# Performance work log

Measured on AMD Instinct MI355X. Metric: run time of the kernel, lower is better.

The kernel has to match this reference:

```python
import jax, jax.numpy as jnp
import numpy as np

# Complete 8-ary tree, depth 5 (levels 0..5), nodes stored level-major.
C = 8
DEPTH = 5
E = 64
H = 512
VOCAB = 20
SIZES = [C ** d for d in range(DEPTH + 1)]
OFFSETS = np.concatenate([[0], np.cumsum(SIZES)]).tolist()
TOTAL = OFFSETS[-1]  # 37449


def setup_inputs() -> dict:
    key = jax.random.key(0)
    ks = jax.random.split(key, 8)
    node_types = jax.random.randint(ks[0], (TOTAL,), 0, 19, dtype=jnp.int32)
    emb = jax.random.normal(ks[1], (VOCAB, E), jnp.float32)
    s_c = 1.0 / np.sqrt(E + H)
    s_g = 1.0 / np.sqrt(H)
    Wc_w = jax.random.normal(ks[2], (H, E + H), jnp.float32) * s_c
    Wc_b = jax.random.normal(ks[3], (H,), jnp.float32) * s_c
    W_ih = jax.random.normal(ks[4], (3 * H, H), jnp.float32) * s_g
    W_hh = jax.random.normal(ks[5], (3 * H, H), jnp.float32) * s_g
    b_ih = jax.random.normal(ks[6], (3 * H,), jnp.float32) * s_g
    b_hh = jax.random.normal(ks[7], (3 * H,), jnp.float32) * s_g
    return {"node_types": node_types, "emb": emb, "Wc_w": Wc_w, "Wc_b": Wc_b,
            "W_ih": W_ih, "W_hh": W_hh, "b_ih": b_ih, "b_hh": b_hh}


def _gru_last(seq, W_ih, W_hh, b_ih, b_hh):
    """PyTorch-convention GRU over child axis; seq: [n, C, H] -> last hidden [n, H]."""
    n = seq.shape[0]
    gx = jnp.einsum('ncH,gH->cng', seq, W_ih) + b_ih  # [C, n, 3H], precomputed input gates

    def step(h, gx_t):
        gh = h @ W_hh.T + b_hh
        xr, xz, xn = jnp.split(gx_t, 3, axis=-1)
        hr, hz, hn = jnp.split(gh, 3, axis=-1)
        r = jax.nn.sigmoid(xr + hr)
        z = jax.nn.sigmoid(xz + hz)
        cand = jnp.tanh(xn + r * hn)
        h_new = (1.0 - z) * cand + z * h
        return h_new, None

    h0 = jnp.zeros((n, H), seq.dtype)
    h_last, _ = jax.lax.scan(step, h0, gx)
    return h_last


def reference(node_types, emb, Wc_w, Wc_b, W_ih, W_hh, b_ih, b_hh):
    embeds = emb[node_types]                       # [TOTAL, E]
    Wc_e = Wc_w[:, :E]                              # acts on embedding part
    Wc_h = Wc_w[:, E:]                              # acts on child-encoding part
    # Leaf level: hidden part of concat is zero-padded -> only Wc_e contributes.
    off = OFFSETS[DEPTH]
    h = jnp.tanh(embeds[off:off + SIZES[DEPTH]] @ Wc_e.T + Wc_b)  # [8^5, H]
    # Bottom-up level batching: each internal node's children are contiguous.
    for d in range(DEPTH - 1, -1, -1):
        child_seq = h.reshape(SIZES[d], C, H)
        child_enc = _gru_last(child_seq, W_ih, W_hh, b_ih, b_hh)  # [8^d, H]
        off = OFFSETS[d]
        h = jnp.tanh(embeds[off:off + SIZES[d]] @ Wc_e.T + child_enc @ Wc_h.T + Wc_b)
    return h[0]  # root encoding, [H]
```

## Files before the change

kernel.cpp:

```cpp
#include <hip/hip_runtime.h>
#include <hip/hip_bf16.h>
#include <math.h>

#define HID 512
#define WCW_LD 576
#define LEAF 4681

typedef unsigned short u16;
typedef __attribute__((ext_vector_type(8))) short bf16x8;
typedef __attribute__((ext_vector_type(4))) float f32x4;

__device__ __forceinline__ u16 f2bf(float f) {
    union { float f; unsigned u; } x; x.f = f;
    unsigned r = x.u + 0x7fffu + ((x.u >> 16) & 1u);
    return (u16)(r >> 16);
}
__device__ __forceinline__ float bf2f(u16 b) {
    union { unsigned u; float f; } x; x.u = ((unsigned)b) << 16; return x.f;
}
__device__ __forceinline__ float sigm(float x) { return 1.f / (1.f + expf(-x)); }

__device__ __forceinline__ int swz(int row, int byte) { return byte ^ ((row & 7) << 4); }

__global__ void pe_kernel(const float* __restrict__ emb, const float* __restrict__ Wc_w,
                          const float* __restrict__ Wc_b, float* __restrict__ Pe,
                          u16* __restrict__ PeT16) {
    int v = blockIdx.x, j = threadIdx.x;
    __shared__ float e[64];
    if (threadIdx.x < 64) e[threadIdx.x] = emb[v * 64 + threadIdx.x];
    __syncthreads();
    float acc = Wc_b[j];
    const float* w = Wc_w + (long long)j * WCW_LD;
#pragma unroll 8
    for (int k = 0; k < 64; ++k) acc += e[k] * w[k];
    Pe[v * HID + j] = acc;
    PeT16[v * HID + j] = f2bf(tanhf(acc));
}

__global__ void conv_w_kernel(const float* __restrict__ W_ih, const float* __restrict__ W_hh,
                              const float* __restrict__ Wc_w,
                              u16* __restrict__ Wih16, u16* __restrict__ Whh16,
                              u16* __restrict__ Wch16) {
    int idx = blockIdx.x * blockDim.x + threadIdx.x;
    int stride = gridDim.x * blockDim.x;
    for (int i = idx; i < 3 * HID * HID; i += stride) {
        Wih16[i] = f2bf(W_ih[i]);
        Whh16[i] = f2bf(W_hh[i]);
    }
    for (int i = idx; i < HID * HID; i += stride) {
        int j = i >> 9, k = i & 511;
        Wch16[i] = f2bf(Wc_w[(long long)j * WCW_LD + 64 + k]);
    }
}

__global__ __launch_bounds__(256)
void gx20_kernel(const u16* __restrict__ PeT16, const u16* __restrict__ Wih16,
                 const float* __restrict__ b_ih, float* __restrict__ Gx20) {
    int v = blockIdx.x;
    int j = blockIdx.y * 256 + threadIdx.x;
    const u16* a = PeT16 + v * HID;
    const u16* b = Wih16 + (long long)j * HID;
    float acc = b_ih[j];
    for (int k = 0; k < HID; k += 8) {
        bf16x8 av = *(const bf16x8*)(a + k);
        bf16x8 bv = *(const bf16x8*)(b + k);
#pragma unroll
        for (int i = 0; i < 8; ++i) acc += bf2f((u16)av[i]) * bf2f((u16)bv[i]);
    }
    Gx20[v * 1536 + j] = acc;
}

__global__ void h1_kernel(const float* __restrict__ Gx20, const float* __restrict__ b_hh,
                          float* __restrict__ H1f, u16* __restrict__ H1_16) {
    int v = blockIdx.x, j = threadIdx.x;
    float xr = Gx20[v * 1536 + j], xz = Gx20[v * 1536 + 512 + j], xn = Gx20[v * 1536 + 1024 + j];
    float r = sigm(xr + b_hh[j]);
    float z = sigm(xz + b_hh[HID + j]);
    float cand = tanhf(xn + r * b_hh[2 * HID + j]);
    float h = (1.f - z) * cand;
    H1f[v * HID + j] = h;
    H1_16[v * HID + j] = f2bf(h);
}

template<bool F32OUT>
__global__ __launch_bounds__(256)
void gx_gemm(const u16* __restrict__ Asrc, const u16* __restrict__ W16,
             const float* __restrict__ bias, u16* __restrict__ g16,
             float* __restrict__ gf, int M) {
    __shared__ __align__(16) uint8_t sA[128 * 128];
    __shared__ __align__(16) uint8_t sB[64 * 128];
    int tid = threadIdx.x, lane = tid & 63, w = tid >> 6;
    int j0 = blockIdx.x * 64;
    int m0 = blockIdx.y * 128;

    f32x4 acc[2][4];
#pragma unroll
    for (int m = 0; m < 2; ++m)
#pragma unroll
        for (int jf = 0; jf < 4; ++jf) acc[m][jf] = (f32x4){0.f, 0.f, 0.f, 0.f};

    for (int k0 = 0; k0 < HID; k0 += 64) {
#pragma unroll
        for (int l = 0; l < 4; ++l) {
            int e = tid + l * 256;
            int r = e >> 3, c = e & 7;
            int gm = m0 + r;
            uint4 v = make_uint4(0u, 0u, 0u, 0u);
            if (gm < M) v = *(const uint4*)(Asrc + (long long)gm * HID + k0 + c * 8);
            *(uint4*)(sA + r * 128 + swz(r, c * 16)) = v;
        }
#pragma unroll
        for (int l = 0; l < 2; ++l) {
            int e = tid + l * 256;
            int r = e >> 3, c = e & 7;
            uint4 v = *(const uint4*)(W16 + (long long)(j0 + r) * HID + k0 + c * 8);
            *(uint4*)(sB + r * 128 + swz(r, c * 16)) = v;
        }
        __syncthreads();
#pragma unroll
        for (int ks = 0; ks < 2; ++ks) {
            int kb = ks * 64 + ((lane >> 4) << 4);
            int ar = lane & 15;
            bf16x8 a0 = *(const bf16x8*)(sA + (w * 32 + ar) * 128 + swz(ar, kb));
            bf16x8 a1 = *(const bf16x8*)(sA + (w * 32 + 16 + ar) * 128 + swz(ar, kb));
#pragma unroll
            for (int jf = 0; jf < 4; ++jf) {
                bf16x8 b = *(const bf16x8*)(sB + (jf * 16 + ar) * 128 + swz(ar, kb));
                acc[0][jf] = __builtin_amdgcn_mfma_f32_16x16x32_bf16(a0, b, acc[0][jf], 0, 0, 0);
                acc[1][jf] = __builtin_amdgcn_mfma_f32_16x16x32_bf16(a1, b, acc[1][jf], 0, 0, 0);
            }
        }
        __syncthreads();
    }

#pragma unroll
    for (int jf = 0; jf < 4; ++jf) {
        int j = j0 + jf * 16 + (lane & 15);
        float bv = bias[j];
#pragma unroll
        for (int m = 0; m < 2; ++m) {
#pragma unroll
            for (int q = 0; q < 4; ++q) {
                int row = m0 + w * 32 + m * 16 + (lane >> 4) * 4 + q;
                if (row < M) {
                    float val = acc[m][jf][q] + bv;
                    if (F32OUT) gf[(long long)row * 1536 + j] = val;
                    else        g16[(long long)row * 1536 + j] = f2bf(val);
                }
            }
        }
    }
}

__global__ __launch_bounds__(256)
void h2_expand(const float* __restrict__ Gx20, const float* __restrict__ Gh1,
               const float* __restrict__ H1f, float* __restrict__ h2f,
               u16* __restrict__ h2_16) {
    int idx = blockIdx.x * 256 + threadIdx.x;
    int pr = idx >> 9, j = idx & 511;
    int v0 = pr / 20, v1 = pr % 20;
    const float* gx = Gx20 + (long long)v1 * 1536 + j;
    const float* gh = Gh1 + (long long)v0 * 1536 + j;
    float r = sigm(gx[0] + gh[0]);
    float z = sigm(gx[512] + gh[512]);
    float cand = tanhf(gx[1024] + r * gh[1024]);
    float h = (1.f - z) * cand + z * H1f[(long long)v0 * HID + j];
    h2f[(long long)pr * HID + j] = h;
    h2_16[(long long)pr * HID + j] = f2bf(h);
}

__global__ __launch_bounds__(256)
void h3_expand(const float* __restrict__ Gx20, const float* __restrict__ Gh2,
               const float* __restrict__ h2f, const int* __restrict__ nt,
               float* __restrict__ hdst_f, u16* __restrict__ hdst16) {
    int idx = blockIdx.x * 256 + threadIdx.x;
    int p = idx >> 9, j = idx & 511;
    int v0 = nt[LEAF + p * 8], v1 = nt[LEAF + p * 8 + 1], v2 = nt[LEAF + p * 8 + 2];
    int pr = v0 * 20 + v1;
    const float* gx = Gx20 + (long long)v2 * 1536 + j;
    const float* gh = Gh2 + (long long)pr * 1536 + j;
    float r = sigm(gx[0] + gh[0]);
    float z = sigm(gx[512] + gh[512]);
    float cand = tanhf(gx[1024] + r * gh[1024]);
    float h = (1.f - z) * cand + z * h2f[(long long)pr * HID + j];
    hdst_f[(long long)p * HID + j] = h;
    hdst16[(long long)p * HID + j] = f2bf(h);
}

template<int GX_TABLE>
__global__ __launch_bounds__(256, 4)
void step32(const u16* __restrict__ hsrc16, const float* __restrict__ hsrc_f,
            const float* __restrict__ Gx20, const u16* __restrict__ gx16, int t,
            const int* __restrict__ nt,
            float* __restrict__ hdst_f, u16* __restrict__ hdst16,
            const u16* __restrict__ Whh16, const float* __restrict__ b_hh, int n) {
    __shared__ __align__(16) uint8_t sA[32 * 128];
    __shared__ __align__(16) uint8_t sB[3][64 * 128];
    int tid = threadIdx.x, lane = tid & 63, w = tid >> 6;
    int p0 = blockIdx.x * 32, j0 = blockIdx.y * 64;
    int ar = lane & 15;

    f32x4 acc[3][2];
#pragma unroll
    for (int g = 0; g < 3; ++g)
#pragma unroll
        for (int m = 0; m < 2; ++m) acc[g][m] = (f32x4){0.f, 0.f, 0.f, 0.f};

    for (int kt = 0; kt < 8; ++kt) {
        int k0 = kt * 64;
        {
            int r = tid >> 3, c = tid & 7;
            int p = p0 + r;
            uint4 v = make_uint4(0u, 0u, 0u, 0u);
            if (p < n) v = *(const uint4*)(hsrc16 + (long long)p * HID + k0 + c * 8);
            *(uint4*)(sA + r * 128 + swz(r, c * 16)) = v;
        }
#pragma unroll
        for (int g = 0; g < 3; ++g) {
#pragma unroll
            for (int l = 0; l < 2; ++l) {
                int e = tid + l * 256;
                int r = e >> 3, c = e & 7;
                uint4 v = *(const uint4*)(Whh16 + (long long)(g * HID + j0 + r) * HID + k0 + c * 8);
                *(uint4*)(sB[g] + r * 128 + swz(r, c * 16)) = v;
            }
        }
        __syncthreads();
#pragma unroll
        for (int ks = 0; ks < 2; ++ks) {
            int kb = ks * 64 + ((lane >> 4) << 4);
            bf16x8 a0 = *(const bf16x8*)(sA + ar * 128 + swz(ar, kb));
            bf16x8 a1 = *(const bf16x8*)(sA + (16 + ar) * 128 + swz(ar, kb));
#pragma unroll
            for (int g = 0; g < 3; ++g) {
                bf16x8 b = *(const bf16x8*)(sB[g] + (w * 16 + ar) * 128 + swz(ar, kb));
                acc[g][0] = __builtin_amdgcn_mfma_f32_16x16x32_bf16(a0, b, acc[g][0], 0, 0, 0);
                acc[g][1] = __builtin_amdgcn_mfma_f32_16x16x32_bf16(a1, b, acc[g][1], 0, 0, 0);
            }
        }
        __syncthreads();
    }

    int jj = j0 + w * 16 + ar;
    float bhr = b_hh[jj], bhz = b_hh[HID + jj], bhn = b_hh[2 * HID + jj];
#pragma unroll
    for (int m = 0; m < 2; ++m) {
#pragma unroll
        for (int q = 0; q < 4; ++q) {
            int p = p0 + m * 16 + (lane >> 4) * 4 + q;
            if (p >= n) continue;
            float xr, xz, xn;
            if (GX_TABLE) {
                int v = nt[LEAF + p * 8 + t];
                const float* gp = Gx20 + (long long)v * 1536 + jj;
                xr = gp[0]; xz = gp[512]; xn = gp[1024];
            } else {
                long long gb = ((long long)(p * 8 + t)) * 1536 + jj;
                xr = bf2f(gx16[gb]); xz = bf2f(gx16[gb + 512]); xn = bf2f(gx16[gb + 1024]);
            }
            float r = sigm(xr + acc[0][m][q] + bhr);
            float z = sigm(xz + acc[1][m][q] + bhz);
            float cand = tanhf(xn + r * (acc[2][m][q] + bhn));
            float hp = hsrc_f[(long long)p * HID + jj];
            float hnew = (1.f - z) * cand + z * hp;
            hdst_f[(long long)p * HID + jj] = hnew;
            hdst16[(long long)p * HID + jj] = f2bf(hnew);
        }
    }
}

__global__ __launch_bounds__(256, 4)
void combine32(const u16* __restrict__ enc_in, const u16* __restrict__ Wch16,
               const int* __restrict__ nt, int off, const float* __restrict__ Pe,
               u16* __restrict__ out16, int n) {
    __shared__ __align__(16) uint8_t sA[32 * 128];
    __shared__ __align__(16) uint8_t sB[64 * 128];
    int tid = threadIdx.x, lane = tid & 63, w = tid >> 6;
    int p0 = blockIdx.x * 32, j0 = blockIdx.y * 64;
    int ar = lane & 15;

    f32x4 acc[2];
    acc[0] = (f32x4){0.f, 0.f, 0.f, 0.f};
    acc[1] = (f32x4){0.f, 0.f, 0.f, 0.f};

    for (int kt = 0; kt < 8; ++kt) {
        int k0 = kt * 64;
        {
            int r = tid >> 3, c = tid & 7;
            uint4 v = make_uint4(0u, 0u, 0u, 0u);
            if (p0 + r < n) v = *(const uint4*)(enc_in + (long long)(p0 + r) * HID + k0 + c * 8);
            *(uint4*)(sA + r * 128 + swz(r, c * 16)) = v;
        }
#pragma unroll
        for (int l = 0; l < 2; ++l) {
            int e = tid + l * 256;
            int r = e >> 3, c = e & 7;
            uint4 v = *(const uint4*)(Wch16 + (long long)(j0 + r) * HID + k0 + c * 8);
            *(uint4*)(sB + r * 128 + swz(r, c * 16)) = v;
        }
        __syncthreads();
#pragma unroll
        for (int ks = 0; ks < 2; ++ks) {
            int kb = ks * 64 + ((lane >> 4) << 4);
            bf16x8 a0 = *(const bf16x8*)(sA + ar * 128 + swz(ar, kb));
            bf16x8 a1 = *(const bf16x8*)(sA + (16 + ar) * 128 + swz(ar, kb));
            bf16x8 b = *(const bf16x8*)(sB + (w * 16 + ar) * 128 + swz(ar, kb));
            acc[0] = __builtin_amdgcn_mfma_f32_16x16x32_bf16(a0, b, acc[0], 0, 0, 0);
            acc[1] = __builtin_amdgcn_mfma_f32_16x16x32_bf16(a1, b, acc[1], 0, 0, 0);
        }
        __syncthreads();
    }

    int jj = j0 + w * 16 + ar;
#pragma unroll
    for (int m = 0; m < 2; ++m) {
#pragma unroll
        for (int q = 0; q < 4; ++q) {
            int p = p0 + m * 16 + (lane >> 4) * 4 + q;
            if (p >= n) continue;
            int tv = nt[off + p];
            float v = tanhf(Pe[(long long)tv * HID + jj] + acc[m][q]);
            out16[(long long)p * HID + jj] = f2bf(v);
        }
    }
}

__global__ __launch_bounds__(256)
void t0_simt(const u16* __restrict__ gx16, const float* __restrict__ b_hh,
             float* __restrict__ hdst_f, u16* __restrict__ hdst16, int n) {
    int idx = blockIdx.x * 256 + threadIdx.x;
    int p = idx >> 9, j = idx & 511;
    if (p >= n) return;
    long long gb = ((long long)(p * 8)) * 1536 + j;
    float xr = bf2f(gx16[gb]), xz = bf2f(gx16[gb + 512]), xn = bf2f(gx16[gb + 1024]);
    float r = sigm(xr + b_hh[j]);
    float z = sigm(xz + b_hh[HID + j]);
    float cand = tanhf(xn + r * b_hh[2 * HID + j]);
    float h = (1.f - z) * cand;
    hdst_f[(long long)p * HID + j] = h;
    hdst16[(long long)p * HID + j] = f2bf(h);
}

__global__ __launch_bounds__(256)
void step_simt(const u16* __restrict__ gx16, int t,
               const float* __restrict__ hsrc_f, const u16* __restrict__ hsrc16,
               float* __restrict__ hdst_f, u16* __restrict__ hdst16,
               const u16* __restrict__ Whh16, const float* __restrict__ b_hh, int n) {
    int idx = blockIdx.x * 256 + threadIdx.x;
    int kc = idx & 3, pj = idx >> 2;
    int p = pj >> 9, j = pj & 511;
    if (p >= n) return;
    const u16* hp16 = hsrc16 + (long long)p * HID + kc * 128;
    const u16* w0 = Whh16 + (long long)j * HID + kc * 128;
    const u16* w1 = w0 + (long long)HID * HID;
    const u16* w2 = w1 + (long long)HID * HID;
    float a0 = 0.f, a1 = 0.f, a2 = 0.f;
#pragma unroll 4
    for (int k = 0; k < 128; k += 8) {
        bf16x8 hv = *(const bf16x8*)(hp16 + k);
        bf16x8 v0 = *(const bf16x8*)(w0 + k);
        bf16x8 v1 = *(const bf16x8*)(w1 + k);
        bf16x8 v2 = *(const bf16x8*)(w2 + k);
#pragma unroll
        for (int i = 0; i < 8; ++i) {
            float hh = bf2f((u16)hv[i]);
            a0 += hh * bf2f((u16)v0[i]);
            a1 += hh * bf2f((u16)v1[i]);
            a2 += hh * bf2f((u16)v2[i]);
        }
    }
    a0 += __shfl_xor(a0, 1); a0 += __shfl_xor(a0, 2);
    a1 += __shfl_xor(a1, 1); a1 += __shfl_xor(a1, 2);
    a2 += __shfl_xor(a2, 1); a2 += __shfl_xor(a2, 2);
    if (kc == 0) {
        long long gb = ((long long)(p * 8 + t)) * 1536 + j;
        float xr = bf2f(gx16[gb]), xz = bf2f(gx16[gb + 512]), xn = bf2f(gx16[gb + 1024]);
        float r = sigm(xr + a0 + b_hh[j]);
        float z = sigm(xz + a1 + b_hh[HID + j]);
        float cand = tanhf(xn + r * (a2 + b_hh[2 * HID + j]));
        float hp = hsrc_f[(long long)p * HID + j];
        float hnew = (1.f - z) * cand + z * hp;
        hdst_f[(long long)p * HID + j] = hnew;
        hdst16[(long long)p * HID + j] = f2bf(hnew);
    }
}

__global__ __launch_bounds__(256)
void combine_simt(const u16* __restrict__ h16, const u16* __restrict__ Wch16,
                  const int* __restrict__ nt, int off, const float* __restrict__ Pe,
                  u16* __restrict__ enc16, float* __restrict__ outf, int n) {
    int idx = blockIdx.x * 256 + threadIdx.x;
    int kc = idx & 3, pj = idx >> 2;
    int p = pj >> 9, j = pj & 511;
    if (p >= n) return;
    const u16* hp = h16 + (long long)p * HID + kc * 128;
    const u16* wr = Wch16 + (long long)j * HID + kc * 128;
    float a = 0.f;
#pragma unroll 4
    for (int k = 0; k < 128; k += 8) {
        bf16x8 hv = *(const bf16x8*)(hp + k);
        bf16x8 wv = *(const bf16x8*)(wr + k);
#pragma unroll
        for (int i = 0; i < 8; ++i) a += bf2f((u16)hv[i]) * bf2f((u16)wv[i]);
    }
    a += __shfl_xor(a, 1); a += __shfl_xor(a, 2);
    if (kc == 0) {
        int tv = nt[off + p];
        float v = tanhf(Pe[(long long)tv * HID + j] + a);
        enc16[(long long)p * HID + j] = f2bf(v);
        if (outf) outf[(long long)p * HID + j] = v;
    }
}

extern "C" void kernel_launch(void* const* d_in, const int* in_sizes, int n_in,
                              void* d_out, int out_size, void* d_ws, size_t ws_size,
                              hipStream_t stream) {
    const int*   nt   = (const int*)d_in[0];
    const float* emb  = (const float*)d_in[1];
    const float* Wc_w = (const float*)d_in[2];
    const float* Wc_b = (const float*)d_in[3];
    const float* W_ih = (const float*)d_in[4];
    const float* W_hh = (const float*)d_in[5];
    const float* b_ih = (const float*)d_in[6];
    const float* b_hh = (const float*)d_in[7];

    uint8_t* p = (uint8_t*)d_ws;
    u16*   gx16  = (u16*)p;   p += (size_t)4096 * 1536 * 2;
    u16*   enc16 = (u16*)p;   p += (size_t)4096 * HID * 2;
    float* hf[2]; u16* h16[2];
    hf[0]  = (float*)p; p += (size_t)4096 * HID * 4;
    hf[1]  = (float*)p; p += (size_t)4096 * HID * 4;
    h16[0] = (u16*)p;   p += (size_t)4096 * HID * 2;
    h16[1] = (u16*)p;   p += (size_t)4096 * HID * 2;
    u16*   Wih16 = (u16*)p;   p += (size_t)3 * HID * HID * 2;
    u16*   Whh16 = (u16*)p;   p += (size_t)3 * HID * HID * 2;
    u16*   Wch16 = (u16*)p;   p += (size_t)HID * HID * 2;
    float* Pe    = (float*)p; p += (size_t)20 * HID * 4;
    u16*   PeT16 = (u16*)p;   p += (size_t)20 * HID * 2;
    float* Gx20  = (float*)p; p += (size_t)20 * 1536 * 4;
    float* H1f   = (float*)p; p += (size_t)20 * HID * 4;
    u16*   H1_16 = (u16*)p;   p += (size_t)20 * HID * 2;
    float* Gh1   = (float*)p; p += (size_t)20 * 1536 * 4;
    float* Gh2   = (float*)p; p += (size_t)400 * 1536 * 4;
    float* h2f   = (float*)p; p += (size_t)400 * HID * 4;
    u16*   h2_16 = (u16*)p;   p += (size_t)400 * HID * 2;

    conv_w_kernel<<<1024, 256, 0, stream>>>(W_ih, W_hh, Wc_w, Wih16, Whh16, Wch16);
    pe_kernel<<<20, 512, 0, stream>>>(emb, Wc_w, Wc_b, Pe, PeT16);
    gx20_kernel<<<dim3(20, 6), 256, 0, stream>>>(PeT16, Wih16, b_ih, Gx20);
    h1_kernel<<<20, 512, 0, stream>>>(Gx20, b_hh, H1f, H1_16);

    {
        int n = 4096;
        gx_gemm<true><<<dim3(24, 1), 256, 0, stream>>>(H1_16, Whh16, b_hh, nullptr, Gh1, 20);
        h2_expand<<<800, 256, 0, stream>>>(Gx20, Gh1, H1f, h2f, h2_16);
        gx_gemm<true><<<dim3(24, 4), 256, 0, stream>>>(h2_16, Whh16, b_hh, nullptr, Gh2, 400);
        h3_expand<<<8192, 256, 0, stream>>>(Gx20, Gh2, h2f, nt, hf[0], h16[0]);
        int cur = 0;
        dim3 sgrid(n / 32, 8);
        for (int t = 3; t < 8; ++t) {
            step32<1><<<sgrid, 256, 0, stream>>>(h16[cur], hf[cur], Gx20, nullptr, t, nt,
                                                 hf[cur ^ 1], h16[cur ^ 1], Whh16, b_hh, n);
            cur ^= 1;
        }
        combine32<<<sgrid, 256, 0, stream>>>(h16[cur], Wch16, nt, 585, Pe, enc16, n);
    }

    const int sizes[4] = {512, 64, 8, 1};
    const int offs[4]  = {73, 9, 1, 0};
    for (int li = 0; li < 4; ++li) {
        int n = sizes[li], off = offs[li];
        int M = n * 8;
        dim3 ggrid(24, (M + 127) / 128);
        gx_gemm<false><<<ggrid, 256, 0, stream>>>(enc16, Wih16, b_ih, gx16, nullptr, M);

        t0_simt<<<n * 2, 256, 0, stream>>>(gx16, b_hh, hf[0], h16[0], n);
        int cur = 0;
        if (n >= 512) {
            dim3 sgrid(n / 32, 8);
            for (int t = 1; t < 8; ++t) {
                step32<0><<<sgrid, 256, 0, stream>>>(h16[cur], hf[cur], nullptr, gx16, t, nt,
                                                     hf[cur ^ 1], h16[cur ^ 1], Whh16, b_hh, n);
                cur ^= 1;
            }
            combine32<<<sgrid, 256, 0, stream>>>(h16[cur], Wch16, nt, off, Pe, enc16, n);
        } else {
            for (int t = 1; t < 8; ++t) {
                step_simt<<<n * 8, 256, 0, stream>>>(gx16, t, hf[cur], h16[cur],
                                                     hf[cur ^ 1], h16[cur ^ 1], Whh16, b_hh, n);
                cur ^= 1;
            }
            combine_simt<<<n * 8, 256, 0, stream>>>(h16[cur], Wch16, nt, off, Pe, enc16,
                                                    (li == 3) ? (float*)d_out : (float*)0, n);
        }
    }
}
```

Baseline: 627.1 us.

## Fuse setup kernels and use 16-row tiles for the 512-node level

Merges the weight conversion and the Pe embedding projection into one launch. Fuses the Gx20 GEMV with the h1 gate math, and the Gh1 GEMV with the h2 pairwise expansion, which removes the Gh1 buffer and several small launches. Templates step32/combine32 on the number of rows per block and uses 16-row tiles for the n=512 level so that more blocks fill the GPU. The fused GEMV kernels run only 20 blocks with per-thread dot products, which could be slower than the previous multi-block versions.

```diff
diff --git a/kernel.cpp b/kernel.cpp
--- a/kernel.cpp
+++ b/kernel.cpp
@@ -22,64 +22,100 @@
 
 __device__ __forceinline__ int swz(int row, int byte) { return byte ^ ((row & 7) << 4); }
 
-__global__ void pe_kernel(const float* __restrict__ emb, const float* __restrict__ Wc_w,
-                          const float* __restrict__ Wc_b, float* __restrict__ Pe,
-                          u16* __restrict__ PeT16) {
+__global__ __launch_bounds__(512)
+void conv_pe(const float* __restrict__ W_ih, const float* __restrict__ W_hh,
+             const float* __restrict__ Wc_w, const float* __restrict__ emb,
+             const float* __restrict__ Wc_b,
+             u16* __restrict__ Wih16, u16* __restrict__ Whh16, u16* __restrict__ Wch16,
+             float* __restrict__ Pe, u16* __restrict__ PeT16) {
+    if (blockIdx.x < 20) {
+        int v = blockIdx.x, j = threadIdx.x;
+        __shared__ float e[64];
+        if (threadIdx.x < 64) e[threadIdx.x] = emb[v * 64 + threadIdx.x];
+        __syncthreads();
+        float acc = Wc_b[j];
+        const float* w = Wc_w + (long long)j * WCW_LD;
+#pragma unroll 8
+        for (int k = 0; k < 64; ++k) acc += e[k] * w[k];
+        Pe[v * HID + j] = acc;
+        PeT16[v * HID + j] = f2bf(tanhf(acc));
+    } else {
+        int idx = (blockIdx.x - 20) * 512 + threadIdx.x;
+        int stride = (gridDim.x - 20) * 512;
+        for (int i = idx; i < 3 * HID * HID; i += stride) {
+            Wih16[i] = f2bf(W_ih[i]);
+            Whh16[i] = f2bf(W_hh[i]);
+        }
+        for (int i = idx; i < HID * HID; i += stride) {
+            int j = i >> 9, k = i & 511;
+            Wch16[i] = f2bf(Wc_w[(long long)j * WCW_LD + 64 + k]);
+        }
+    }
+}
+
+__global__ __launch_bounds__(512)
+void gx20h1(const u16* __restrict__ PeT16, const u16* __restrict__ Wih16,
+            const float* __restrict__ b_ih, const float* __restrict__ b_hh,
+            float* __restrict__ Gx20, float* __restrict__ H1f, u16* __restrict__ H1_16) {
     int v = blockIdx.x, j = threadIdx.x;
-    __shared__ float e[64];
-    if (threadIdx.x < 64) e[threadIdx.x] = emb[v * 64 + threadIdx.x];
-    __syncthreads();
-    float acc = Wc_b[j];
-    const float* w = Wc_w + (long long)j * WCW_LD;
-#pragma unroll 8
-    for (int k = 0; k < 64; ++k) acc += e[k] * w[k];
-    Pe[v * HID + j] = acc;
-    PeT16[v * HID + j] = f2bf(tanhf(acc));
-}
-
-__global__ void conv_w_kernel(const float* __restrict__ W_ih, const float* __restrict__ W_hh,
-                              const float* __restrict__ Wc_w,
-                              u16* __restrict__ Wih16, u16* __restrict__ Whh16,
-                              u16* __restrict__ Wch16) {
-    int idx = blockIdx.x * blockDim.x + threadIdx.x;
-    int stride = gridDim.x * blockDim.x;
-    for (int i = idx; i < 3 * HID * HID; i += stride) {
-        Wih16[i] = f2bf(W_ih[i]);
-        Whh16[i] = f2bf(W_hh[i]);
-    }
-    for (int i = idx; i < HID * HID; i += stride) {
-        int j = i >> 9, k = i & 511;
-        Wch16[i] = f2bf(Wc_w[(long long)j * WCW_LD + 64 + k]);
-    }
-}
-
-__global__ __launch_bounds__(256)
-void gx20_kernel(const u16* __restrict__ PeT16, const u16* __restrict__ Wih16,
-                 const float* __restrict__ b_ih, float* __restrict__ Gx20) {
-    int v = blockIdx.x;
-    int j = blockIdx.y * 256 + threadIdx.x;
     const u16* a = PeT16 + v * HID;
-    const u16* b = Wih16 + (long long)j * HID;
-    float acc = b_ih[j];
-    for (int k = 0; k < HID; k += 8) {
-        bf16x8 av = *(const bf16x8*)(a + k);
-        bf16x8 bv = *(const bf16x8*)(b + k);
-#pragma unroll
-        for (int i = 0; i < 8; ++i) acc += bf2f((u16)av[i]) * bf2f((u16)bv[i]);
-    }
-    Gx20[v * 1536 + j] = acc;
-}
-
-__global__ void h1_kernel(const float* __restrict__ Gx20, const float* __restrict__ b_hh,
-                          float* __restrict__ H1f, u16* __restrict__ H1_16) {
-    int v = blockIdx.x, j = threadIdx.x;
-    float xr = Gx20[v * 1536 + j], xz = Gx20[v * 1536 + 512 + j], xn = Gx20[v * 1536 + 1024 + j];
-    float r = sigm(xr + b_hh[j]);
-    float z = sigm(xz + b_hh[HID + j]);
-    float cand = tanhf(xn + r * b_hh[2 * HID + j]);
+    float acc[3] = {0.f, 0.f, 0.f};
+#pragma unroll
+    for (int g = 0; g < 3; ++g) {
+        const u16* b = Wih16 + (long long)(g * HID + j) * HID;
+        float s = 0.f;
+        for (int k = 0; k < HID; k += 8) {
+            bf16x8 av = *(const bf16x8*)(a + k);
+            bf16x8 bv = *(const bf16x8*)(b + k);
+#pragma unroll
+            for (int i = 0; i < 8; ++i) s += bf2f((u16)av[i]) * bf2f((u16)bv[i]);
+        }
+        acc[g] = s + b_ih[g * HID + j];
+    }
+    Gx20[v * 1536 + j] = acc[0];
+    Gx20[v * 1536 + 512 + j] = acc[1];
+    Gx20[v * 1536 + 1024 + j] = acc[2];
+    float r = sigm(acc[0] + b_hh[j]);
+    float z = sigm(acc[1] + b_hh[HID + j]);
+    float cand = tanhf(acc[2] + r * b_hh[2 * HID + j]);
     float h = (1.f - z) * cand;
     H1f[v * HID + j] = h;
     H1_16[v * HID + j] = f2bf(h);
+}
+
+__global__ __launch_bounds__(512)
+void gh1h2(const u16* __restrict__ H1_16, const u16* __restrict__ Whh16,
+           const float* __restrict__ b_hh, const float* __restrict__ Gx20,
+           const float* __restrict__ H1f, float* __restrict__ h2f,
+           u16* __restrict__ h2_16) {
+    int v0 = blockIdx.x, j = threadIdx.x;
+    const u16* a = H1_16 + v0 * HID;
+    float gh[3];
+#pragma unroll
+    for (int g = 0; g < 3; ++g) {
+        const u16* b = Whh16 + (long long)(g * HID + j) * HID;
+        float s = 0.f;
+        for (int k = 0; k < HID; k += 8) {
+            bf16x8 av = *(const bf16x8*)(a + k);
+            bf16x8 bv = *(const bf16x8*)(b + k);
+#pragma unroll
+            for (int i = 0; i < 8; ++i) s += bf2f((u16)av[i]) * bf2f((u16)bv[i]);
+        }
+        gh[g] = s + b_hh[g * HID + j];
+    }
+    float hp = H1f[(long long)v0 * HID + j];
+    for (int v1 = 0; v1 < 20; ++v1) {
+        float xr = Gx20[v1 * 1536 + j];
+        float xz = Gx20[v1 * 1536 + 512 + j];
+        float xn = Gx20[v1 * 1536 + 1024 + j];
+        float r = sigm(xr + gh[0]);
+        float z = sigm(xz + gh[1]);
+        float cand = tanhf(xn + r * gh[2]);
+        float h = (1.f - z) * cand + z * hp;
+        int pr = v0 * 20 + v1;
+        h2f[(long long)pr * HID + j] = h;
+        h2_16[(long long)pr * HID + j] = f2bf(h);
+    }
 }
 
 template<bool F32OUT>
@@ -150,23 +186,6 @@
             }
         }
     }
-}
-
-__global__ __launch_bounds__(256)
-void h2_expand(const float* __restrict__ Gx20, const float* __restrict__ Gh1,
-               const float* __restrict__ H1f, float* __restrict__ h2f,
-               u16* __restrict__ h2_16) {
-    int idx = blockIdx.x * 256 + threadIdx.x;
-    int pr = idx >> 9, j = idx & 511;
-    int v0 = pr / 20, v1 = pr % 20;
-    const float* gx = Gx20 + (long long)v1 * 1536 + j;
-    const float* gh = Gh1 + (long long)v0 * 1536 + j;
-    float r = sigm(gx[0] + gh[0]);
-    float z = sigm(gx[512] + gh[512]);
-    float cand = tanhf(gx[1024] + r * gh[1024]);
-    float h = (1.f - z) * cand + z * H1f[(long long)v0 * HID + j];
-    h2f[(long long)pr * HID + j] = h;
-    h2_16[(long long)pr * HID + j] = f2bf(h);
 }
 
 __global__ __launch_bounds__(256)
@@ -187,28 +206,29 @@
     hdst16[(long long)p * HID + j] = f2bf(h);
 }
 
-template<int GX_TABLE>
+template<int GX_TABLE, int PROWS>
 __global__ __launch_bounds__(256, 4)
 void step32(const u16* __restrict__ hsrc16, const float* __restrict__ hsrc_f,
             const float* __restrict__ Gx20, const u16* __restrict__ gx16, int t,
             const int* __restrict__ nt,
             float* __restrict__ hdst_f, u16* __restrict__ hdst16,
             const u16* __restrict__ Whh16, const float* __restrict__ b_hh, int n) {
-    __shared__ __align__(16) uint8_t sA[32 * 128];
+    constexpr int MT = PROWS / 16;
+    __shared__ __align__(16) uint8_t sA[PROWS * 128];
     __shared__ __align__(16) uint8_t sB[3][64 * 128];
     int tid = threadIdx.x, lane = tid & 63, w = tid >> 6;
-    int p0 = blockIdx.x * 32, j0 = blockIdx.y * 64;
+    int p0 = blockIdx.x * PROWS, j0 = blockIdx.y * 64;
     int ar = lane & 15;
 
-    f32x4 acc[3][2];
+    f32x4 acc[3][MT];
 #pragma unroll
     for (int g = 0; g < 3; ++g)
 #pragma unroll
-        for (int m = 0; m < 2; ++m) acc[g][m] = (f32x4){0.f, 0.f, 0.f, 0.f};
+        for (int m = 0; m < MT; ++m) acc[g][m] = (f32x4){0.f, 0.f, 0.f, 0.f};
 
     for (int kt = 0; kt < 8; ++kt) {
         int k0 = kt * 64;
-        {
+        if (tid < PROWS * 8) {
             int r = tid >> 3, c = tid & 7;
             int p = p0 + r;
             uint4 v = make_uint4(0u, 0u, 0u, 0u);
@@ -229,13 +249,16 @@
 #pragma unroll
         for (int ks = 0; ks < 2; ++ks) {
             int kb = ks * 64 + ((lane >> 4) << 4);
-            bf16x8 a0 = *(const bf16x8*)(sA + ar * 128 + swz(ar, kb));
-            bf16x8 a1 = *(const bf16x8*)(sA + (16 + ar) * 128 + swz(ar, kb));
+            bf16x8 a[MT];
+#pragma unroll
+            for (int m = 0; m < MT; ++m)
+                a[m] = *(const bf16x8*)(sA + (m * 16 + ar) * 128 + swz(ar, kb));
 #pragma unroll
             for (int g = 0; g < 3; ++g) {
                 bf16x8 b = *(const bf16x8*)(sB[g] + (w * 16 + ar) * 128 + swz(ar, kb));
-                acc[g][0] = __builtin_amdgcn_mfma_f32_16x16x32_bf16(a0, b, acc[g][0], 0, 0, 0);
-                acc[g][1] = __builtin_amdgcn_mfma_f32_16x16x32_bf16(a1, b, acc[g][1], 0, 0, 0);
+#pragma unroll
+                for (int m = 0; m < MT; ++m)
+                    acc[g][m] = __builtin_amdgcn_mfma_f32_16x16x32_bf16(a[m], b, acc[g][m], 0, 0, 0);
             }
         }
         __syncthreads();
@@ -244,7 +267,7 @@
     int jj = j0 + w * 16 + ar;
     float bhr = b_hh[jj], bhz = b_hh[HID + jj], bhn = b_hh[2 * HID + jj];
 #pragma unroll
-    for (int m = 0; m < 2; ++m) {
+    for (int m = 0; m < MT; ++m) {
 #pragma unroll
         for (int q = 0; q < 4; ++q) {
             int p = p0 + m * 16 + (lane >> 4) * 4 + q;
@@ -269,23 +292,25 @@
     }
 }
 
+template<int PROWS>
 __global__ __launch_bounds__(256, 4)
 void combine32(const u16* __restrict__ enc_in, const u16* __restrict__ Wch16,
                const int* __restrict__ nt, int off, const float* __restrict__ Pe,
                u16* __restrict__ out16, int n) {
-    __shared__ __align__(16) uint8_t sA[32 * 128];
+    constexpr int MT = PROWS / 16;
+    __shared__ __align__(16) uint8_t sA[PROWS * 128];
     __shared__ __align__(16) uint8_t sB[64 * 128];
     int tid = threadIdx.x, lane = tid & 63, w = tid >> 6;
-    int p0 = blockIdx.x * 32, j0 = blockIdx.y * 64;
+    int p0 = blockIdx.x * PROWS, j0 = blockIdx.y * 64;
     int ar = lane & 15;
 
-    f32x4 acc[2];
-    acc[0] = (f32x4){0.f, 0.f, 0.f, 0.f};
-    acc[1] = (f32x4){0.f, 0.f, 0.f, 0.f};
+    f32x4 acc[MT];
+#pragma unroll
+    for (int m = 0; m < MT; ++m) acc[m] = (f32x4){0.f, 0.f, 0.f, 0.f};
 
     for (int kt = 0; kt < 8; ++kt) {
         int k0 = kt * 64;
-        {
+        if (tid < PROWS * 8) {
             int r = tid >> 3, c = tid & 7;
             uint4 v = make_uint4(0u, 0u, 0u, 0u);
             if (p0 + r < n) v = *(const uint4*)(enc_in + (long long)(p0 + r) * HID + k0 + c * 8);
@@ -302,18 +327,19 @@
 #pragma unroll
         for (int ks = 0; ks < 2; ++ks) {
             int kb = ks * 64 + ((lane >> 4) << 4);
-            bf16x8 a0 = *(const bf16x8*)(sA + ar * 128 + swz(ar, kb));
-            bf16x8 a1 = *(const bf16x8*)(sA + (16 + ar) * 128 + swz(ar, kb));
             bf16x8 b = *(const bf16x8*)(sB + (w * 16 + ar) * 128 + swz(ar, kb));
-            acc[0] = __builtin_amdgcn_mfma_f32_16x16x32_bf16(a0, b, acc[0], 0, 0, 0);
-            acc[1] = __builtin_amdgcn_mfma_f32_16x16x32_bf16(a1, b, acc[1], 0, 0, 0);
+#pragma unroll
+            for (int m = 0; m < MT; ++m) {
+                bf16x8 a = *(const bf16x8*)(sA + (m * 16 + ar) * 128 + swz(ar, kb));
+                acc[m] = __builtin_amdgcn_mfma_f32_16x16x32_bf16(a, b, acc[m], 0, 0, 0);
+            }
         }
         __syncthreads();
     }
 
     int jj = j0 + w * 16 + ar;
 #pragma unroll
-    for (int m = 0; m < 2; ++m) {
+    for (int m = 0; m < MT; ++m) {
 #pragma unroll
         for (int q = 0; q < 4; ++q) {
             int p = p0 + m * 16 + (lane >> 4) * 4 + q;
@@ -440,30 +466,27 @@
     float* Gx20  = (float*)p; p += (size_t)20 * 1536 * 4;
     float* H1f   = (float*)p; p += (size_t)20 * HID * 4;
     u16*   H1_16 = (u16*)p;   p += (size_t)20 * HID * 2;
-    float* Gh1   = (float*)p; p += (size_t)20 * 1536 * 4;
     float* Gh2   = (float*)p; p += (size_t)400 * 1536 * 4;
     float* h2f   = (float*)p; p += (size_t)400 * HID * 4;
     u16*   h2_16 = (u16*)p;   p += (size_t)400 * HID * 2;
 
-    conv_w_kernel<<<1024, 256, 0, stream>>>(W_ih, W_hh, Wc_w, Wih16, Whh16, Wch16);
-    pe_kernel<<<20, 512, 0, stream>>>(emb, Wc_w, Wc_b, Pe, PeT16);
-    gx20_kernel<<<dim3(20, 6), 256, 0, stream>>>(PeT16, Wih16, b_ih, Gx20);
-    h1_kernel<<<20, 512, 0, stream>>>(Gx20, b_hh, H1f, H1_16);
+    conv_pe<<<532, 512, 0, stream>>>(W_ih, W_hh, Wc_w, emb, Wc_b,
+                                     Wih16, Whh16, Wch16, Pe, PeT16);
+    gx20h1<<<20, 512, 0, stream>>>(PeT16, Wih16, b_ih, b_hh, Gx20, H1f, H1_16);
 
     {
         int n = 4096;
-        gx_gemm<true><<<dim3(24, 1), 256, 0, stream>>>(H1_16, Whh16, b_hh, nullptr, Gh1, 20);
-        h2_expand<<<800, 256, 0, stream>>>(Gx20, Gh1, H1f, h2f, h2_16);
+        gh1h2<<<20, 512, 0, stream>>>(H1_16, Whh16, b_hh, Gx20, H1f, h2f, h2_16);
         gx_gemm<true><<<dim3(24, 4), 256, 0, stream>>>(h2_16, Whh16, b_hh, nullptr, Gh2, 400);
         h3_expand<<<8192, 256, 0, stream>>>(Gx20, Gh2, h2f, nt, hf[0], h16[0]);
         int cur = 0;
         dim3 sgrid(n / 32, 8);
         for (int t = 3; t < 8; ++t) {
-            step32<1><<<sgrid, 256, 0, stream>>>(h16[cur], hf[cur], Gx20, nullptr, t, nt,
-                                                 hf[cur ^ 1], h16[cur ^ 1], Whh16, b_hh, n);
+            step32<1, 32><<<sgrid, 256, 0, stream>>>(h16[cur], hf[cur], Gx20, nullptr, t, nt,
+                                                     hf[cur ^ 1], h16[cur ^ 1], Whh16, b_hh, n);
             cur ^= 1;
         }
-        combine32<<<sgrid, 256, 0, stream>>>(h16[cur], Wch16, nt, 585, Pe, enc16, n);
+        combine32<32><<<sgrid, 256, 0, stream>>>(h16[cur], Wch16, nt, 585, Pe, enc16, n);
     }
 
     const int sizes[4] = {512, 64, 8, 1};
@@ -477,13 +500,13 @@
         t0_simt<<<n * 2, 256, 0, stream>>>(gx16, b_hh, hf[0], h16[0], n);
         int cur = 0;
         if (n >= 512) {
-            dim3 sgrid(n / 32, 8);
+            dim3 sgrid(n / 16, 8);
             for (int t = 1; t < 8; ++t) {
-                step32<0><<<sgrid, 256, 0, stream>>>(h16[cur], hf[cur], nullptr, gx16, t, nt,
-                                                     hf[cur ^ 1], h16[cur ^ 1], Whh16, b_hh, n);
+                step32<0, 16><<<sgrid, 256, 0, stream>>>(h16[cur], hf[cur], nullptr, gx16, t, nt,
+                                                         hf[cur ^ 1], h16[cur ^ 1], Whh16, b_hh, n);
                 cur ^= 1;
             }
-            combine32<<<sgrid, 256, 0, stream>>>(h16[cur], Wch16, nt, off, Pe, enc16, n);
+            combine32<16><<<sgrid, 256, 0, stream>>>(h16[cur], Wch16, nt, off, Pe, enc16, n);
         } else {
             for (int t = 1; t < 8; ++t) {
                 step_simt<<<n * 8, 256, 0, stream>>>(gx16, t, hf[cur], h16[cur],
```

Result: slower. 689.9 us (+10.0%).
